# Kernel optimization log

Measured on AMD Instinct MI355X. Metric: run time of the kernel, lower is better.

Reference implementation:

```python
import jax, jax.numpy as jnp
import numpy as np

B, LA, LQ, LO, H, OUT = 32, 2048, 64, 32, 1024, 5


def _kaiming(key, out_f, in_f):
    return jax.random.normal(key, (out_f, in_f), jnp.float32) * np.sqrt(2.0 / in_f)


def setup_inputs() -> dict:
    key = jax.random.key(0)
    ks = jax.random.split(key, 16)
    inp = {
        "article_contexts": jax.random.normal(ks[0], (B, LA, H), jnp.float32),
        "question_contexts": jax.random.normal(ks[1], (B, LQ, H), jnp.float32),
        "options_embeds": jax.random.normal(ks[2], (B, 5, LO, H), jnp.float32),
        "answer_indices": jax.random.randint(ks[3], (B,), 0, LQ),
    }
    # mlp_att (article-question attention) params
    inp["a_Qw"], inp["a_Qb"] = _kaiming(ks[4], H, H), jnp.zeros((H,), jnp.float32)
    inp["a_Kw"], inp["a_Kb"] = _kaiming(ks[5], H, H), jnp.zeros((H,), jnp.float32)
    inp["a_Vw"], inp["a_Vb"] = _kaiming(ks[6], H, H), jnp.zeros((H,), jnp.float32)
    inp["a_vw"], inp["a_vb"] = _kaiming(ks[7], 1, H), jnp.zeros((1,), jnp.float32)
    # dot_layer (option attention) params
    inp["d_Qw"], inp["d_Qb"] = _kaiming(ks[8], H, H), jnp.zeros((H,), jnp.float32)
    inp["d_Kw"], inp["d_Kb"] = _kaiming(ks[9], H, H), jnp.zeros((H,), jnp.float32)
    inp["d_Vw"], inp["d_Vb"] = _kaiming(ks[10], H, H), jnp.zeros((H,), jnp.float32)
    inp["d_vw"], inp["d_vb"] = _kaiming(ks[11], 1, H), jnp.zeros((1,), jnp.float32)
    # final linear: hidden_size*5 -> output_dim
    inp["f_w"], inp["f_b"] = _kaiming(ks[12], OUT, 5 * H), jnp.zeros((OUT,), jnp.float32)
    return inp


def _mlp_att(Q, K, V, Qw, Qb, Kw, Kb, Vw, Vb, vw, vb):
    # Q: [B, H]; K, V: [B, (..opt..), L, H]. Dropout is identity (eval mode).
    Qp = Q @ Qw.T + Qb                      # [B, H]
    Kp = K @ Kw.T + Kb                      # [..., L, H]
    Vp = V @ Vw.T + Vb                      # [..., L, H]
    while Qp.ndim < Kp.ndim:
        Qp = Qp[..., None, :]
    M = jnp.tanh(Qp + Kp)                   # [..., L, H]
    scores = jax.nn.softmax(M @ vw.T + vb, axis=-2)  # softmax over L, [..., L, 1]
    return jnp.sum(Vp * scores, axis=-2)    # [..., H]


def reference(article_contexts, question_contexts, options_embeds, answer_indices,
              a_Qw, a_Qb, a_Kw, a_Kb, a_Vw, a_Vb, a_vw, a_vb,
              d_Qw, d_Qb, d_Kw, d_Kb, d_Vw, d_Vb, d_vw, d_vb,
              f_w, f_b):
    b = article_contexts.shape[0]
    # gather question context at the answer index -> [B, H]
    oqc = question_contexts[jnp.arange(b), answer_indices]
    # article-question additive attention -> [B, H]
    aq = _mlp_att(oqc, article_contexts, article_contexts,
                  a_Qw, a_Qb, a_Kw, a_Kb, a_Vw, a_Vb, a_vw, a_vb)
    # per-option additive attention, vectorized over the 5 options -> [B, 5, H]
    feats = _mlp_att(aq, options_embeds, options_embeds,
                     d_Qw, d_Qb, d_Kw, d_Kb, d_Vw, d_Vb, d_vw, d_vb)
    # concat options along feature dim, final linear -> [B, OUT]
    logits = feats.reshape(b, -1) @ f_w.T + f_b
    return logits
```

## Files before the change

kernel.cpp:

```cpp
#include <hip/hip_runtime.h>
#include <hip/hip_bf16.h>
#include <math.h>

#define HDIM 1024
#define NB 32
#define LA 2048
#define LO 32

typedef __attribute__((ext_vector_type(8))) short bf16x8;
typedef __attribute__((ext_vector_type(4))) float f32x4;
typedef unsigned int u32;

__device__ __forceinline__ float tanh_fast(float x){
    return 2.0f / (1.0f + __expf(-2.0f * x)) - 1.0f;
}

__device__ __forceinline__ void load_lds16(const void* gptr, void* lptr){
    __builtin_amdgcn_global_load_lds(
        (const __attribute__((address_space(1))) u32*)gptr,
        (__attribute__((address_space(3))) u32*)lptr, 16, 0, 0);
}

__global__ void zero_kernel(float* __restrict__ p, int n){
    int i = blockIdx.x * blockDim.x + threadIdx.x;
    int stride = gridDim.x * blockDim.x;
    for (; i < n; i += stride) p[i] = 0.0f;
}

__global__ void conv_bf16_kernel(const float* __restrict__ in, __hip_bfloat16* __restrict__ out, long n){
    long i = ((long)blockIdx.x * blockDim.x + threadIdx.x) * 4;
    long stride = (long)gridDim.x * blockDim.x * 4;
    for (; i < n; i += stride){
        float4 v = *(const float4*)(in + i);
        union { __hip_bfloat16 h[4]; short4 s; } u;
        u.h[0] = __float2bfloat16(v.x); u.h[1] = __float2bfloat16(v.y);
        u.h[2] = __float2bfloat16(v.z); u.h[3] = __float2bfloat16(v.w);
        *(short4*)(out + i) = u.s;
    }
}

__global__ void gather_kernel(const float* __restrict__ qc, const int* __restrict__ ans,
                              float* __restrict__ oqc){
    int b = blockIdx.x, tid = threadIdx.x;
    int idx = ans[b];
    const float* src = qc + ((size_t)b * 64 + idx) * HDIM;
    float* dst = oqc + (size_t)b * HDIM;
    #pragma unroll
    for (int l = 0; l < 4; l++) dst[tid + l * 256] = src[tid + l * 256];
}

__global__ __launch_bounds__(256) void proj_kernel(
    const float* __restrict__ in, const float* __restrict__ W,
    const float* __restrict__ bias, float* __restrict__ out){
    __shared__ float xin[HDIM];
    const int g = blockIdx.x, tid = threadIdx.x;
    const int lane = tid & 63, wave = tid >> 6;
    *(float4*)&xin[tid * 4] = *(const float4*)&in[(size_t)g * HDIM + tid * 4];
    __syncthreads();
    float4 xv[4];
    #pragma unroll
    for (int c = 0; c < 4; c++) xv[c] = *(const float4*)&xin[(c * 64 + lane) * 4];
    const int hbase = blockIdx.y * 64 + wave * 16;
    #pragma unroll 4
    for (int r = 0; r < 16; r++){
        int h = hbase + r;
        const float* Wr = W + (size_t)h * HDIM;
        float p = 0.f;
        #pragma unroll
        for (int c = 0; c < 4; c++){
            float4 wv = *(const float4*)&Wr[(c * 64 + lane) * 4];
            p = fmaf(xv[c].x, wv.x, p); p = fmaf(xv[c].y, wv.y, p);
            p = fmaf(xv[c].z, wv.z, p); p = fmaf(xv[c].w, wv.w, p);
        }
        #pragma unroll
        for (int off = 1; off < 64; off <<= 1) p += __shfl_xor(p, off, 64);
        if (lane == 0) out[(size_t)g * HDIM + h] = p + bias[h];
    }
}

#define NT 32
__global__ __launch_bounds__(512, 4) void score_mfma_kA(
    const __hip_bfloat16* __restrict__ X, const __hip_bfloat16* __restrict__ Kw,
    const float* __restrict__ Kb, const float* __restrict__ Qp,
    const float* __restrict__ vw, float* __restrict__ s,
    int row_off, int rows_per_batch)
{
    __shared__ __align__(16) char lds[49152];
    const int tid = threadIdx.x;
    const int lane = tid & 63, wid = tid >> 6;
    const int wm = wid >> 2, wn = wid & 3;
    const int lr = lane & 15, lg = lane >> 4;

    const int na = gridDim.x >> 3;
    const int per = na >> 3;
    const int bid = blockIdx.x;
    const int xcd = bid & 7, seq = bid >> 3;
    const int a_idx = xcd * per + (seq >> 3);
    const int h_idx = seq & 7;
    const int a0 = a_idx * 256;
    const int h0 = h_idx * 128;

    f32x4 acc[4][4] = {};

    const int rA  = tid >> 2;
    const int kcA = ((tid & 3) ^ ((rA >> 1) & 3)) * 16;
    const int rB1 = rA + 128;
    const char* pA  = (const char*)Kw + (size_t)(h0 + rA) * 2048 + kcA;
    const char* pB0 = (const char*)X  + (size_t)(a0 + rA) * 2048 + kcA;
    const char* pB1 = (const char*)X  + (size_t)(a0 + rB1) * 2048 + kcA;
    char* dA  = lds + tid * 16;
    char* dB0 = lds + 8192 + tid * 16;
    char* dB1 = lds + 16384 + tid * 16;

    int aoff[4], boff[4];
    #pragma unroll
    for (int hf = 0; hf < 4; hf++){
        int rw = wm * 64 + hf * 16 + lr;
        aoff[hf] = rw * 64 + ((lg * 16) ^ (((rw >> 1) & 3) << 4));
    }
    #pragma unroll
    for (int af = 0; af < 4; af++){
        int rw = wn * 64 + af * 16 + lr;
        boff[af] = 8192 + rw * 64 + ((lg * 16) ^ (((rw >> 1) & 3) << 4));
    }

#define STAGE_ADV(bufoff) do { \
    load_lds16(pA,  dA  + (bufoff)); \
    load_lds16(pB0, dB0 + (bufoff)); \
    load_lds16(pB1, dB1 + (bufoff)); \
    pA += 64; pB0 += 64; pB1 += 64; } while(0)

#define COMPUTE(bufoff) do { \
    bf16x8 av[4], bv[4]; \
    _Pragma("unroll") \
    for (int hf = 0; hf < 4; hf++) \
        av[hf] = *(const bf16x8*)(lds + (bufoff) + aoff[hf]); \
    _Pragma("unroll") \
    for (int af = 0; af < 4; af++) \
        bv[af] = *(const bf16x8*)(lds + (bufoff) + boff[af]); \
    __builtin_amdgcn_s_setprio(1); \
    _Pragma("unroll") \
    for (int hf = 0; hf < 4; hf++) \
        _Pragma("unroll") \
        for (int af = 0; af < 4; af++) \
            acc[hf][af] = __builtin_amdgcn_mfma_f32_16x16x32_bf16(av[hf], bv[af], acc[hf][af], 0, 0, 0); \
    __builtin_amdgcn_s_setprio(0); } while(0)

    STAGE_ADV(0);
    STAGE_ADV(24576);
    int bo = 0;
    for (int kt = 0; kt < NT - 1; ++kt){
        asm volatile("s_waitcnt vmcnt(3)" ::: "memory");
        __builtin_amdgcn_s_barrier();
        __builtin_amdgcn_sched_barrier(0);
        COMPUTE(bo);
        __builtin_amdgcn_s_barrier();
        if (kt < NT - 2) STAGE_ADV(bo);
        bo ^= 24576;
    }
    asm volatile("s_waitcnt vmcnt(0)" ::: "memory");
    __builtin_amdgcn_s_barrier();
    __builtin_amdgcn_sched_barrier(0);
    COMPUTE(bo);

    const int b = (row_off + a0) / rows_per_batch;
    float qv[4][4], vv[4][4];
    #pragma unroll
    for (int hf = 0; hf < 4; hf++){
        int hbase = h0 + wm * 64 + hf * 16 + lg * 4;
        float4 kb4 = *(const float4*)(Kb + hbase);
        float4 qp4 = *(const float4*)(Qp + (size_t)b * HDIM + hbase);
        float4 vw4 = *(const float4*)(vw + hbase);
        qv[hf][0] = kb4.x + qp4.x; qv[hf][1] = kb4.y + qp4.y;
        qv[hf][2] = kb4.z + qp4.z; qv[hf][3] = kb4.w + qp4.w;
        vv[hf][0] = vw4.x; vv[hf][1] = vw4.y; vv[hf][2] = vw4.z; vv[hf][3] = vw4.w;
    }
    #pragma unroll
    for (int af = 0; af < 4; af++){
        float sacc = 0.f;
        #pragma unroll
        for (int hf = 0; hf < 4; hf++)
            #pragma unroll
            for (int r = 0; r < 4; r++)
                sacc += tanh_fast(acc[hf][af][r] + qv[hf][r]) * vv[hf][r];
        sacc += __shfl_xor(sacc, 16, 64);
        sacc += __shfl_xor(sacc, 32, 64);
        if (lane < 16)
            atomicAdd(&s[row_off + a0 + wn * 64 + af * 16 + lr], sacc);
    }
#undef STAGE_ADV
#undef COMPUTE
}

#define SBM 128
#define SBN 128
__global__ __launch_bounds__(256) void score_mfma_kernel(
    const __hip_bfloat16* __restrict__ X, const __hip_bfloat16* __restrict__ Kw,
    const float* __restrict__ Kb, const float* __restrict__ Qp,
    const float* __restrict__ vw, float* __restrict__ s,
    int row_off, int rows_per_batch)
{
    __shared__ __align__(16) __hip_bfloat16 As[SBM][32];
    __shared__ __align__(16) __hip_bfloat16 Bs[SBN][32];
    const int tid = threadIdx.x;
    const int lane = tid & 63, wid = tid >> 6;
    const int wm = wid >> 1, wn = wid & 1;
    const int row0 = blockIdx.x * SBM;
    const int h0 = blockIdx.y * SBN;
    const int lr = lane & 15, lg = lane >> 4;

    f32x4 acc[4][4] = {};

    for (int k0 = 0; k0 < HDIM; k0 += 32){
        #pragma unroll
        for (int l = 0; l < 2; l++){
            int f = tid + l * 256;
            int r = f >> 2, c8 = (f & 3) * 8;
            load_lds16(X + (size_t)(row0 + r) * HDIM + k0 + c8, &As[0][0] + f * 8);
            load_lds16(Kw + (size_t)(h0 + r) * HDIM + k0 + c8, &Bs[0][0] + f * 8);
        }
        __syncthreads();
        bf16x8 a[4], b[4];
        #pragma unroll
        for (int i = 0; i < 4; i++)
            a[i] = *(const bf16x8*)&As[wm * 64 + i * 16 + lr][lg * 8];
        #pragma unroll
        for (int j = 0; j < 4; j++)
            b[j] = *(const bf16x8*)&Bs[wn * 64 + j * 16 + lr][lg * 8];
        #pragma unroll
        for (int i = 0; i < 4; i++)
            #pragma unroll
            for (int j = 0; j < 4; j++)
                acc[i][j] = __builtin_amdgcn_mfma_f32_16x16x32_bf16(a[i], b[j], acc[i][j], 0, 0, 0);
        __syncthreads();
    }

    float kbv[4], vwv[4];
    #pragma unroll
    for (int j = 0; j < 4; j++){
        int h = h0 + wn * 64 + j * 16 + lr;
        kbv[j] = Kb[h]; vwv[j] = vw[h];
    }
    #pragma unroll
    for (int i = 0; i < 4; i++){
        #pragma unroll
        for (int reg = 0; reg < 4; reg++){
            int r = row0 + wm * 64 + i * 16 + lg * 4 + reg;
            int gr = row_off + r;
            int bb = gr / rows_per_batch;
            const float* Qpb = Qp + (size_t)bb * HDIM;
            float p = 0.f;
            #pragma unroll
            for (int j = 0; j < 4; j++){
                int h = h0 + wn * 64 + j * 16 + lr;
                p += tanh_fast(acc[i][j][reg] + kbv[j] + Qpb[h]) * vwv[j];
            }
            #pragma unroll
            for (int off = 1; off < 16; off <<= 1) p += __shfl_xor(p, off, 16);
            if (lr == 0) atomicAdd(&s[gr], p);
        }
    }
}

__global__ void softmax_kernel(float* __restrict__ s, int Rg){
    __shared__ float red[4];
    int g = blockIdx.x, tid = threadIdx.x;
    float* sg = s + (size_t)g * Rg;
    float m = -INFINITY;
    for (int i = tid; i < Rg; i += 256) m = fmaxf(m, sg[i]);
    #pragma unroll
    for (int off = 32; off > 0; off >>= 1) m = fmaxf(m, __shfl_down(m, off, 64));
    if ((tid & 63) == 0) red[tid >> 6] = m;
    __syncthreads();
    m = fmaxf(fmaxf(red[0], red[1]), fmaxf(red[2], red[3]));
    __syncthreads();
    float sum = 0.f;
    for (int i = tid; i < Rg; i += 256){ float e = __expf(sg[i] - m); sg[i] = e; sum += e; }
    #pragma unroll
    for (int off = 32; off > 0; off >>= 1) sum += __shfl_down(sum, off, 64);
    if ((tid & 63) == 0) red[tid >> 6] = sum;
    __syncthreads();
    float inv = 1.0f / (red[0] + red[1] + red[2] + red[3]);
    for (int i = tid; i < Rg; i += 256) sg[i] *= inv;
}

__global__ void wsum_kernel(const float* __restrict__ X, const float* __restrict__ sc,
                            float* __restrict__ out, int Rg, int rowsPerChunk){
    __shared__ float scs[256];
    int g = blockIdx.x >> 2;
    int kc = blockIdx.x & 3;
    int i0 = blockIdx.y * rowsPerChunk;
    int tid = threadIdx.x;
    if (tid < rowsPerChunk) scs[tid] = sc[(size_t)g * Rg + i0 + tid];
    __syncthreads();
    int k = kc * 256 + tid;
    const float* Xg = X + ((size_t)g * Rg + i0) * HDIM + k;
    float acc = 0.f;
    for (int i = 0; i < rowsPerChunk; i++)
        acc += scs[i] * Xg[(size_t)i * HDIM];
    atomicAdd(&out[(size_t)g * HDIM + k], acc);
}

__global__ void wsum_bf16_kernel(const __hip_bfloat16* __restrict__ X, const float* __restrict__ sc,
                                 float* __restrict__ out, int Rg, int rowsPerChunk){
    __shared__ float scs[256];
    int g = blockIdx.x >> 2;
    int kc = blockIdx.x & 3;
    int i0 = blockIdx.y * rowsPerChunk;
    int tid = threadIdx.x;
    if (tid < rowsPerChunk) scs[tid] = sc[(size_t)g * Rg + i0 + tid];
    __syncthreads();
    int k = kc * 256 + tid;
    const __hip_bfloat16* Xg = X + ((size_t)g * Rg + i0) * HDIM + k;
    float acc = 0.f;
    for (int i = 0; i < rowsPerChunk; i++)
        acc += scs[i] * __bfloat162float(Xg[(size_t)i * HDIM]);
    atomicAdd(&out[(size_t)g * HDIM + k], acc);
}

__global__ void final_kernel(const float* __restrict__ feats, const float* __restrict__ fw,
                             const float* __restrict__ fb, float* __restrict__ out){
    __shared__ float red[4];
    int b = blockIdx.x, tid = threadIdx.x;
    const float* fe = feats + (size_t)b * 5120;
    for (int j = 0; j < 5; j++){
        float acc = 0.f;
        for (int i = tid; i < 5120; i += 256) acc += fe[i] * fw[(size_t)j * 5120 + i];
        #pragma unroll
        for (int off = 32; off > 0; off >>= 1) acc += __shfl_down(acc, off, 64);
        if ((tid & 63) == 0) red[tid >> 6] = acc;
        __syncthreads();
        if (tid == 0) out[b * 5 + j] = fb[j] + red[0] + red[1] + red[2] + red[3];
        __syncthreads();
    }
}

extern "C" void kernel_launch(void* const* d_in, const int* in_sizes, int n_in,
                              void* d_out, int out_size, void* d_ws, size_t ws_size,
                              hipStream_t stream) {
    const float* article  = (const float*)d_in[0];
    const float* question = (const float*)d_in[1];
    const float* options  = (const float*)d_in[2];
    const int*   ans      = (const int*)d_in[3];
    const float* a_Qw = (const float*)d_in[4];  const float* a_Qb = (const float*)d_in[5];
    const float* a_Kw = (const float*)d_in[6];  const float* a_Kb = (const float*)d_in[7];
    const float* a_Vw = (const float*)d_in[8];  const float* a_Vb = (const float*)d_in[9];
    const float* a_vw = (const float*)d_in[10];
    const float* d_Qw = (const float*)d_in[12]; const float* d_Qb = (const float*)d_in[13];
    const float* d_Kw = (const float*)d_in[14]; const float* d_Kb = (const float*)d_in[15];
    const float* d_Vw = (const float*)d_in[16]; const float* d_Vb = (const float*)d_in[17];
    const float* d_vw = (const float*)d_in[18];
    const float* f_w  = (const float*)d_in[20]; const float* f_b  = (const float*)d_in[21];
    float* out = (float*)d_out;

    float* ws = (float*)d_ws;
    float* oqc   = ws;
    float* qp_a  = ws + 32768;
    float* aq    = ws + 65536;
    float* qp_d  = ws + 98304;
    float* feats = ws + 131072;
    float* s_art = ws + 294912;
    float* s_opt = ws + 360448;
    float* w_art = ws + 365568;
    float* wd    = ws + 398336;
    __hip_bfloat16* kwa_bf = (__hip_bfloat16*)(ws + 562176);
    __hip_bfloat16* kwd_bf = kwa_bf + 1048576;
    __hip_bfloat16* opt_bf = kwd_bf + 1048576;
    __hip_bfloat16* art_bf = opt_bf + 5242880;
    size_t used_bytes = 562176 * 4 + (size_t)(1048576 * 2 + 5242880) * 2;
    long avail_rows = (long)((ws_size - used_bytes) / (HDIM * 2));
    int rows_total = NB * LA;
    int chunk_rows = (int)(avail_rows < rows_total ? avail_rows : rows_total);
    chunk_rows &= ~2047;
    if (chunk_rows < 2048) chunk_rows = 2048;

    zero_kernel<<<256, 256, 0, stream>>>(s_art, 267264);
    gather_kernel<<<NB, 256, 0, stream>>>(question, ans, oqc);
    proj_kernel<<<dim3(NB, 16), 256, 0, stream>>>(oqc, a_Qw, a_Qb, qp_a);
    conv_bf16_kernel<<<64, 256, 0, stream>>>(a_Kw, kwa_bf, 1048576);

    for (int r0 = 0; r0 < rows_total; r0 += chunk_rows){
        int nr = rows_total - r0; if (nr > chunk_rows) nr = chunk_rows;
        conv_bf16_kernel<<<1024, 256, 0, stream>>>(article + (size_t)r0 * HDIM, art_bf, (long)nr * HDIM);
        score_mfma_kA<<<(nr / 256) * 8, 512, 0, stream>>>(
            art_bf, kwa_bf, a_Kb, qp_a, a_vw, s_art, r0, LA);
    }
    softmax_kernel<<<NB, 256, 0, stream>>>(s_art, LA);
    if (chunk_rows >= rows_total)
        wsum_bf16_kernel<<<dim3(NB * 4, 8), 256, 0, stream>>>(art_bf, s_art, w_art, LA, 256);
    else
        wsum_kernel<<<dim3(NB * 4, 8), 256, 0, stream>>>(article, s_art, w_art, LA, 256);
    proj_kernel<<<dim3(NB, 16), 256, 0, stream>>>(w_art, a_Vw, a_Vb, aq);

    proj_kernel<<<dim3(NB, 16), 256, 0, stream>>>(aq, d_Qw, d_Qb, qp_d);
    conv_bf16_kernel<<<64, 256, 0, stream>>>(d_Kw, kwd_bf, 1048576);
    conv_bf16_kernel<<<320, 256, 0, stream>>>(options, opt_bf, 5242880);
    score_mfma_kernel<<<dim3((NB * 5 * LO) / SBM, HDIM / SBN), 256, 0, stream>>>(
        opt_bf, kwd_bf, d_Kb, qp_d, d_vw, s_opt, 0, 5 * LO);
    softmax_kernel<<<NB * 5, 256, 0, stream>>>(s_opt, LO);
    wsum_kernel<<<dim3(NB * 5 * 4, 1), 256, 0, stream>>>(options, s_opt, wd, LO, LO);
    proj_kernel<<<dim3(NB * 5, 16), 256, 0, stream>>>(wd, d_Vw, d_Vb, feats);
    final_kernel<<<NB, 256, 0, stream>>>(feats, f_w, f_b, out);
}
```

Measured before the change: 446.2 us.

## Enlarge article score GEMM tile to 256x256 with deeper 8-phase pipelined LDS staging

The article-score MFMA kernel now computes 256 hidden by 256 row tiles per block instead of 128 by 256, halving the grid and the number of times each article row is re-read from global memory. The K loop is restructured into a multi-stage, 8-phase schedule over 128 KB of LDS. Loads for two 32-wide k slabs are interleaved with split LDS reads and MFMA groups, with fine-grained vmcnt waits and barriers. This raises arithmetic intensity and overlaps loads with compute, at the cost of more registers, more LDS, fewer resident blocks per CU, and a more fragile hand-tuned schedule.

After: 439.4 us. Within noise of the previous version (-1.5%).

```diff
diff --git a/kernel.cpp b/kernel.cpp
--- a/kernel.cpp
+++ b/kernel.cpp
@@ -78,118 +78,144 @@
     }
 }
 
-#define NT 32
-__global__ __launch_bounds__(512, 4) void score_mfma_kA(
+__global__ __launch_bounds__(512, 2) void score_mfma8p(
     const __hip_bfloat16* __restrict__ X, const __hip_bfloat16* __restrict__ Kw,
     const float* __restrict__ Kb, const float* __restrict__ Qp,
     const float* __restrict__ vw, float* __restrict__ s,
     int row_off, int rows_per_batch)
 {
-    __shared__ __align__(16) char lds[49152];
+    __shared__ __align__(16) char lds[131072];
     const int tid = threadIdx.x;
     const int lane = tid & 63, wid = tid >> 6;
     const int wm = wid >> 2, wn = wid & 3;
     const int lr = lane & 15, lg = lane >> 4;
 
-    const int na = gridDim.x >> 3;
-    const int per = na >> 3;
+    const int na = gridDim.x >> 2;
     const int bid = blockIdx.x;
     const int xcd = bid & 7, seq = bid >> 3;
-    const int a_idx = xcd * per + (seq >> 3);
-    const int h_idx = seq & 7;
-    const int a0 = a_idx * 256;
-    const int h0 = h_idx * 128;
-
-    f32x4 acc[4][4] = {};
-
-    const int rA  = tid >> 2;
-    const int kcA = ((tid & 3) ^ ((rA >> 1) & 3)) * 16;
-    const int rB1 = rA + 128;
-    const char* pA  = (const char*)Kw + (size_t)(h0 + rA) * 2048 + kcA;
-    const char* pB0 = (const char*)X  + (size_t)(a0 + rA) * 2048 + kcA;
-    const char* pB1 = (const char*)X  + (size_t)(a0 + rB1) * 2048 + kcA;
-    char* dA  = lds + tid * 16;
-    char* dB0 = lds + 8192 + tid * 16;
-    char* dB1 = lds + 16384 + tid * 16;
-
-    int aoff[4], boff[4];
-    #pragma unroll
-    for (int hf = 0; hf < 4; hf++){
-        int rw = wm * 64 + hf * 16 + lr;
+    const int a_idx = xcd * (na >> 3) + (seq >> 2);
+    const int h_idx = seq & 3;
+    const int a0 = a_idx * 256, h0 = h_idx * 256;
+
+    f32x4 acc[8][4] = {};
+    bf16x8 av[8], bv[4];
+
+    const int rA = tid >> 2;
+    const int csw = ((tid & 3) * 16) ^ (((rA >> 1) & 3) << 4);
+    const char* pA = (const char*)Kw + (size_t)(h0 + rA) * 2048 + csw;
+    const char* pB = (const char*)X  + (size_t)(a0 + rA) * 2048 + csw;
+    char* dst0 = lds + tid * 16;
+
+    int aoff[8], boff[4];
+    #pragma unroll
+    for (int hf = 0; hf < 8; hf++){
+        int rw = wm * 128 + hf * 16 + lr;
         aoff[hf] = rw * 64 + ((lg * 16) ^ (((rw >> 1) & 3) << 4));
     }
     #pragma unroll
     for (int af = 0; af < 4; af++){
         int rw = wn * 64 + af * 16 + lr;
-        boff[af] = 8192 + rw * 64 + ((lg * 16) ^ (((rw >> 1) & 3) << 4));
-    }
-
-#define STAGE_ADV(bufoff) do { \
-    load_lds16(pA,  dA  + (bufoff)); \
-    load_lds16(pB0, dB0 + (bufoff)); \
-    load_lds16(pB1, dB1 + (bufoff)); \
-    pA += 64; pB0 += 64; pB1 += 64; } while(0)
-
-#define COMPUTE(bufoff) do { \
-    bf16x8 av[4], bv[4]; \
+        boff[af] = 16384 + rw * 64 + ((lg * 16) ^ (((rw >> 1) & 3) << 4));
+    }
+
+#define ISSUE(P, KOFF, SLOT, PLANE) do { \
+    load_lds16((P) + (KOFF), dst0 + (SLOT) + (PLANE)); \
+    load_lds16((P) + (KOFF) + 262144, dst0 + (SLOT) + (PLANE) + 8192); } while(0)
+#define READS_A(BASE) do { \
     _Pragma("unroll") \
-    for (int hf = 0; hf < 4; hf++) \
-        av[hf] = *(const bf16x8*)(lds + (bufoff) + aoff[hf]); \
+    for (int hf = 0; hf < 8; hf++) av[hf] = *(const bf16x8*)(lds + (BASE) + aoff[hf]); \
+    bv[0] = *(const bf16x8*)(lds + (BASE) + boff[0]); \
+    bv[1] = *(const bf16x8*)(lds + (BASE) + boff[1]); } while(0)
+#define READS_B(BASE) do { \
+    bv[2] = *(const bf16x8*)(lds + (BASE) + boff[2]); \
+    bv[3] = *(const bf16x8*)(lds + (BASE) + boff[3]); } while(0)
+#define MFMA2(A0, A1) do { __builtin_amdgcn_s_setprio(1); \
     _Pragma("unroll") \
-    for (int af = 0; af < 4; af++) \
-        bv[af] = *(const bf16x8*)(lds + (bufoff) + boff[af]); \
-    __builtin_amdgcn_s_setprio(1); \
-    _Pragma("unroll") \
-    for (int hf = 0; hf < 4; hf++) \
-        _Pragma("unroll") \
-        for (int af = 0; af < 4; af++) \
-            acc[hf][af] = __builtin_amdgcn_mfma_f32_16x16x32_bf16(av[hf], bv[af], acc[hf][af], 0, 0, 0); \
+    for (int hf = 0; hf < 8; hf++){ \
+        acc[hf][A0] = __builtin_amdgcn_mfma_f32_16x16x32_bf16(av[hf], bv[A0], acc[hf][A0], 0, 0, 0); \
+        acc[hf][A1] = __builtin_amdgcn_mfma_f32_16x16x32_bf16(av[hf], bv[A1], acc[hf][A1], 0, 0, 0); } \
     __builtin_amdgcn_s_setprio(0); } while(0)
-
-    STAGE_ADV(0);
-    STAGE_ADV(24576);
-    int bo = 0;
-    for (int kt = 0; kt < NT - 1; ++kt){
-        asm volatile("s_waitcnt vmcnt(3)" ::: "memory");
-        __builtin_amdgcn_s_barrier();
-        __builtin_amdgcn_sched_barrier(0);
-        COMPUTE(bo);
-        __builtin_amdgcn_s_barrier();
-        if (kt < NT - 2) STAGE_ADV(bo);
-        bo ^= 24576;
-    }
-    asm volatile("s_waitcnt vmcnt(0)" ::: "memory");
-    __builtin_amdgcn_s_barrier();
-    __builtin_amdgcn_sched_barrier(0);
-    COMPUTE(bo);
+#define BAR() __builtin_amdgcn_s_barrier()
+
+    ISSUE(pA, 0, 0, 0);        ISSUE(pB, 0, 0, 16384);
+    ISSUE(pA, 64, 0, 32768);   ISSUE(pB, 64, 0, 49152);
+    ISSUE(pA, 128, 65536, 0);  ISSUE(pB, 128, 65536, 16384);
+
+    for (int t = 0; t < 14; ++t){
+        const int st = (t & 1) << 16;
+        const int so = st ^ 65536;
+        const int kb = t * 128;
+        ISSUE(pA, kb + 192, so, 32768);
+        asm volatile("s_waitcnt vmcnt(10)" ::: "memory");
+        BAR();
+        READS_A(st);
+        BAR();
+        MFMA2(0, 1);
+        ISSUE(pB, kb + 192, so, 49152);
+        READS_B(st);
+        BAR();
+        MFMA2(2, 3);
+        ISSUE(pA, kb + 256, st, 0);
+        asm volatile("s_waitcnt vmcnt(10)" ::: "memory");
+        BAR();
+        READS_A(st + 32768);
+        BAR();
+        MFMA2(0, 1);
+        ISSUE(pB, kb + 256, st, 16384);
+        READS_B(st + 32768);
+        BAR();
+        MFMA2(2, 3);
+    }
+    {
+        ISSUE(pA, 14 * 128 + 192, 65536, 32768);
+        asm volatile("s_waitcnt vmcnt(10)" ::: "memory");
+        BAR(); READS_A(0); BAR(); MFMA2(0, 1);
+        ISSUE(pB, 14 * 128 + 192, 65536, 49152);
+        READS_B(0); BAR(); MFMA2(2, 3);
+        asm volatile("s_waitcnt vmcnt(8)" ::: "memory");
+        BAR(); READS_A(32768); BAR(); MFMA2(0, 1);
+        READS_B(32768); BAR(); MFMA2(2, 3);
+    }
+    {
+        asm volatile("s_waitcnt vmcnt(4)" ::: "memory");
+        BAR(); READS_A(65536); BAR(); MFMA2(0, 1);
+        READS_B(65536); BAR(); MFMA2(2, 3);
+        asm volatile("s_waitcnt vmcnt(0)" ::: "memory");
+        BAR(); READS_A(65536 + 32768); BAR(); MFMA2(0, 1);
+        READS_B(65536 + 32768); BAR(); MFMA2(2, 3);
+    }
 
     const int b = (row_off + a0) / rows_per_batch;
-    float qv[4][4], vv[4][4];
-    #pragma unroll
-    for (int hf = 0; hf < 4; hf++){
-        int hbase = h0 + wm * 64 + hf * 16 + lg * 4;
+    float part[4] = {0.f, 0.f, 0.f, 0.f};
+    #pragma unroll
+    for (int hf = 0; hf < 8; hf++){
+        int hbase = h0 + wm * 128 + hf * 16 + lg * 4;
         float4 kb4 = *(const float4*)(Kb + hbase);
         float4 qp4 = *(const float4*)(Qp + (size_t)b * HDIM + hbase);
         float4 vw4 = *(const float4*)(vw + hbase);
-        qv[hf][0] = kb4.x + qp4.x; qv[hf][1] = kb4.y + qp4.y;
-        qv[hf][2] = kb4.z + qp4.z; qv[hf][3] = kb4.w + qp4.w;
-        vv[hf][0] = vw4.x; vv[hf][1] = vw4.y; vv[hf][2] = vw4.z; vv[hf][3] = vw4.w;
+        float q0v = kb4.x + qp4.x, q1v = kb4.y + qp4.y;
+        float q2v = kb4.z + qp4.z, q3v = kb4.w + qp4.w;
+        #pragma unroll
+        for (int af = 0; af < 4; af++){
+            part[af] += tanh_fast(acc[hf][af][0] + q0v) * vw4.x;
+            part[af] += tanh_fast(acc[hf][af][1] + q1v) * vw4.y;
+            part[af] += tanh_fast(acc[hf][af][2] + q2v) * vw4.z;
+            part[af] += tanh_fast(acc[hf][af][3] + q3v) * vw4.w;
+        }
     }
     #pragma unroll
     for (int af = 0; af < 4; af++){
-        float sacc = 0.f;
-        #pragma unroll
-        for (int hf = 0; hf < 4; hf++)
-            #pragma unroll
-            for (int r = 0; r < 4; r++)
-                sacc += tanh_fast(acc[hf][af][r] + qv[hf][r]) * vv[hf][r];
-        sacc += __shfl_xor(sacc, 16, 64);
-        sacc += __shfl_xor(sacc, 32, 64);
+        float p = part[af];
+        p += __shfl_xor(p, 16, 64);
+        p += __shfl_xor(p, 32, 64);
         if (lane < 16)
-            atomicAdd(&s[row_off + a0 + wn * 64 + af * 16 + lr], sacc);
-    }
-#undef STAGE_ADV
-#undef COMPUTE
+            atomicAdd(&s[row_off + a0 + wn * 64 + af * 16 + lr], p);
+    }
+#undef ISSUE
+#undef READS_A
+#undef READS_B
+#undef MFMA2
+#undef BAR
 }
 
 #define SBM 128
@@ -382,7 +408,7 @@
     for (int r0 = 0; r0 < rows_total; r0 += chunk_rows){
         int nr = rows_total - r0; if (nr > chunk_rows) nr = chunk_rows;
         conv_bf16_kernel<<<1024, 256, 0, stream>>>(article + (size_t)r0 * HDIM, art_bf, (long)nr * HDIM);
-        score_mfma_kA<<<(nr / 256) * 8, 512, 0, stream>>>(
+        score_mfma8p<<<(nr / 256) * 4, 512, 0, stream>>>(
             art_bf, kwa_bf, a_Kb, qp_a, a_vw, s_art, r0, LA);
     }
     softmax_kernel<<<NB, 256, 0, stream>>>(s_art, LA);
```

## Fuse fp32-to-bf16 article conversion into score MFMA kernel load path

Applied to the files above, without the earlier changes.

The article score GEMM now reads fp32 activations directly, converting them to bf16 in registers and writing them to swizzled LDS. This replaces the separate conversion pass and the bf16 staging buffer. The aim is to avoid writing and re-reading a 128MB bf16 copy and to drop the chunking loop. The trade-off is that B loads go through registers with a full vmcnt(0) wait each iteration instead of async direct-to-LDS loads, which weakens the pipelining. wsum also now reads fp32 from the article instead of the bf16 copy, which doubles its read traffic.

New measurement: 490.0 us. +9.8%, slower.

```diff
diff --git a/kernel.cpp b/kernel.cpp
--- a/kernel.cpp
+++ b/kernel.cpp
@@ -79,11 +79,11 @@
 }
 
 #define NT 32
-__global__ __launch_bounds__(512, 4) void score_mfma_kA(
-    const __hip_bfloat16* __restrict__ X, const __hip_bfloat16* __restrict__ Kw,
+__global__ __launch_bounds__(512, 4) void score_mfma_f32b(
+    const float* __restrict__ Xf, const __hip_bfloat16* __restrict__ Kw,
     const float* __restrict__ Kb, const float* __restrict__ Qp,
     const float* __restrict__ vw, float* __restrict__ s,
-    int row_off, int rows_per_batch)
+    int rows_per_batch)
 {
     __shared__ __align__(16) char lds[49152];
     const int tid = threadIdx.x;
@@ -92,25 +92,25 @@
     const int lr = lane & 15, lg = lane >> 4;
 
     const int na = gridDim.x >> 3;
-    const int per = na >> 3;
     const int bid = blockIdx.x;
     const int xcd = bid & 7, seq = bid >> 3;
-    const int a_idx = xcd * per + (seq >> 3);
+    const int a_idx = xcd * (na >> 3) + (seq >> 3);
     const int h_idx = seq & 7;
-    const int a0 = a_idx * 256;
-    const int h0 = h_idx * 128;
+    const int a0 = a_idx * 256, h0 = h_idx * 128;
 
     f32x4 acc[4][4] = {};
 
-    const int rA  = tid >> 2;
-    const int kcA = ((tid & 3) ^ ((rA >> 1) & 3)) * 16;
-    const int rB1 = rA + 128;
-    const char* pA  = (const char*)Kw + (size_t)(h0 + rA) * 2048 + kcA;
-    const char* pB0 = (const char*)X  + (size_t)(a0 + rA) * 2048 + kcA;
-    const char* pB1 = (const char*)X  + (size_t)(a0 + rB1) * 2048 + kcA;
-    char* dA  = lds + tid * 16;
-    char* dB0 = lds + 8192 + tid * 16;
-    char* dB1 = lds + 16384 + tid * 16;
+    const int rA = tid >> 2;
+    const int srcbA = ((tid & 3) * 16) ^ (((rA >> 1) & 3) << 4);
+    const char* pA = (const char*)Kw + (size_t)(h0 + rA) * 2048 + srcbA;
+    char* dA = lds + tid * 16;
+
+    const int rB = tid >> 1;
+    const int hb = tid & 1;
+    const float* pB = Xf + (size_t)(a0 + rB) * HDIM + hb * 16;
+    const int swzB = ((rB >> 1) & 3) << 4;
+    char* dB0 = lds + 8192 + rB * 64 + ((hb * 32) ^ swzB);
+    char* dB1 = lds + 8192 + rB * 64 + ((hb * 32 + 16) ^ swzB);
 
     int aoff[4], boff[4];
     #pragma unroll
@@ -124,20 +124,29 @@
         boff[af] = 8192 + rw * 64 + ((lg * 16) ^ (((rw >> 1) & 3) << 4));
     }
 
-#define STAGE_ADV(bufoff) do { \
-    load_lds16(pA,  dA  + (bufoff)); \
-    load_lds16(pB0, dB0 + (bufoff)); \
-    load_lds16(pB1, dB1 + (bufoff)); \
-    pA += 64; pB0 += 64; pB1 += 64; } while(0)
-
+    float4 br0, br1, br2, br3;
+#define LOADB(kt) do { const float* q = pB + (kt) * 32; \
+    br0 = *(const float4*)q; br1 = *(const float4*)(q + 4); \
+    br2 = *(const float4*)(q + 8); br3 = *(const float4*)(q + 12); } while(0)
+#define CVTWRITE(bufoff) do { \
+    union { __hip_bfloat16 h[8]; bf16x8 v; } u0, u1; \
+    u0.h[0]=__float2bfloat16(br0.x); u0.h[1]=__float2bfloat16(br0.y); \
+    u0.h[2]=__float2bfloat16(br0.z); u0.h[3]=__float2bfloat16(br0.w); \
+    u0.h[4]=__float2bfloat16(br1.x); u0.h[5]=__float2bfloat16(br1.y); \
+    u0.h[6]=__float2bfloat16(br1.z); u0.h[7]=__float2bfloat16(br1.w); \
+    u1.h[0]=__float2bfloat16(br2.x); u1.h[1]=__float2bfloat16(br2.y); \
+    u1.h[2]=__float2bfloat16(br2.z); u1.h[3]=__float2bfloat16(br2.w); \
+    u1.h[4]=__float2bfloat16(br3.x); u1.h[5]=__float2bfloat16(br3.y); \
+    u1.h[6]=__float2bfloat16(br3.z); u1.h[7]=__float2bfloat16(br3.w); \
+    *(bf16x8*)(dB0 + (bufoff)) = u0.v; \
+    *(bf16x8*)(dB1 + (bufoff)) = u1.v; } while(0)
+#define ISSUEA(kt, bufoff) load_lds16(pA + (size_t)(kt) * 64, dA + (bufoff))
 #define COMPUTE(bufoff) do { \
     bf16x8 av[4], bv[4]; \
     _Pragma("unroll") \
-    for (int hf = 0; hf < 4; hf++) \
-        av[hf] = *(const bf16x8*)(lds + (bufoff) + aoff[hf]); \
+    for (int hf = 0; hf < 4; hf++) av[hf] = *(const bf16x8*)(lds + (bufoff) + aoff[hf]); \
     _Pragma("unroll") \
-    for (int af = 0; af < 4; af++) \
-        bv[af] = *(const bf16x8*)(lds + (bufoff) + boff[af]); \
+    for (int af = 0; af < 4; af++) bv[af] = *(const bf16x8*)(lds + (bufoff) + boff[af]); \
     __builtin_amdgcn_s_setprio(1); \
     _Pragma("unroll") \
     for (int hf = 0; hf < 4; hf++) \
@@ -146,24 +155,28 @@
             acc[hf][af] = __builtin_amdgcn_mfma_f32_16x16x32_bf16(av[hf], bv[af], acc[hf][af], 0, 0, 0); \
     __builtin_amdgcn_s_setprio(0); } while(0)
 
-    STAGE_ADV(0);
-    STAGE_ADV(24576);
+    ISSUEA(0, 0);
+    LOADB(0);
+    CVTWRITE(0);
+    asm volatile("s_waitcnt vmcnt(0)" ::: "memory");
+    __syncthreads();
+
     int bo = 0;
-    for (int kt = 0; kt < NT - 1; ++kt){
-        asm volatile("s_waitcnt vmcnt(3)" ::: "memory");
-        __builtin_amdgcn_s_barrier();
-        __builtin_amdgcn_sched_barrier(0);
+    for (int t = 0; t < NT; ++t){
+        if (t < NT - 1){
+            ISSUEA(t + 1, bo ^ 24576);
+            LOADB(t + 1);
+        }
         COMPUTE(bo);
-        __builtin_amdgcn_s_barrier();
-        if (kt < NT - 2) STAGE_ADV(bo);
+        if (t < NT - 1){
+            CVTWRITE(bo ^ 24576);
+            asm volatile("s_waitcnt vmcnt(0)" ::: "memory");
+        }
+        __syncthreads();
         bo ^= 24576;
     }
-    asm volatile("s_waitcnt vmcnt(0)" ::: "memory");
-    __builtin_amdgcn_s_barrier();
-    __builtin_amdgcn_sched_barrier(0);
-    COMPUTE(bo);
-
-    const int b = (row_off + a0) / rows_per_batch;
+
+    const int b = a0 / rows_per_batch;
     float qv[4][4], vv[4][4];
     #pragma unroll
     for (int hf = 0; hf < 4; hf++){
@@ -186,9 +199,11 @@
         sacc += __shfl_xor(sacc, 16, 64);
         sacc += __shfl_xor(sacc, 32, 64);
         if (lane < 16)
-            atomicAdd(&s[row_off + a0 + wn * 64 + af * 16 + lr], sacc);
-    }
-#undef STAGE_ADV
+            atomicAdd(&s[a0 + wn * 64 + af * 16 + lr], sacc);
+    }
+#undef LOADB
+#undef CVTWRITE
+#undef ISSUEA
 #undef COMPUTE
 }
 
@@ -298,23 +313,6 @@
     float acc = 0.f;
     for (int i = 0; i < rowsPerChunk; i++)
         acc += scs[i] * Xg[(size_t)i * HDIM];
-    atomicAdd(&out[(size_t)g * HDIM + k], acc);
-}
-
-__global__ void wsum_bf16_kernel(const __hip_bfloat16* __restrict__ X, const float* __restrict__ sc,
-                                 float* __restrict__ out, int Rg, int rowsPerChunk){
-    __shared__ float scs[256];
-    int g = blockIdx.x >> 2;
-    int kc = blockIdx.x & 3;
-    int i0 = blockIdx.y * rowsPerChunk;
-    int tid = threadIdx.x;
-    if (tid < rowsPerChunk) scs[tid] = sc[(size_t)g * Rg + i0 + tid];
-    __syncthreads();
-    int k = kc * 256 + tid;
-    const __hip_bfloat16* Xg = X + ((size_t)g * Rg + i0) * HDIM + k;
-    float acc = 0.f;
-    for (int i = 0; i < rowsPerChunk; i++)
-        acc += scs[i] * __bfloat162float(Xg[(size_t)i * HDIM]);
     atomicAdd(&out[(size_t)g * HDIM + k], acc);
 }
 
@@ -366,30 +364,16 @@
     __hip_bfloat16* kwa_bf = (__hip_bfloat16*)(ws + 562176);
     __hip_bfloat16* kwd_bf = kwa_bf + 1048576;
     __hip_bfloat16* opt_bf = kwd_bf + 1048576;
-    __hip_bfloat16* art_bf = opt_bf + 5242880;
-    size_t used_bytes = 562176 * 4 + (size_t)(1048576 * 2 + 5242880) * 2;
-    long avail_rows = (long)((ws_size - used_bytes) / (HDIM * 2));
-    int rows_total = NB * LA;
-    int chunk_rows = (int)(avail_rows < rows_total ? avail_rows : rows_total);
-    chunk_rows &= ~2047;
-    if (chunk_rows < 2048) chunk_rows = 2048;
 
     zero_kernel<<<256, 256, 0, stream>>>(s_art, 267264);
     gather_kernel<<<NB, 256, 0, stream>>>(question, ans, oqc);
     proj_kernel<<<dim3(NB, 16), 256, 0, stream>>>(oqc, a_Qw, a_Qb, qp_a);
     conv_bf16_kernel<<<64, 256, 0, stream>>>(a_Kw, kwa_bf, 1048576);
 
-    for (int r0 = 0; r0 < rows_total; r0 += chunk_rows){
-        int nr = rows_total - r0; if (nr > chunk_rows) nr = chunk_rows;
-        conv_bf16_kernel<<<1024, 256, 0, stream>>>(article + (size_t)r0 * HDIM, art_bf, (long)nr * HDIM);
-        score_mfma_kA<<<(nr / 256) * 8, 512, 0, stream>>>(
-            art_bf, kwa_bf, a_Kb, qp_a, a_vw, s_art, r0, LA);
-    }
+    score_mfma_f32b<<<(NB * LA / 256) * 8, 512, 0, stream>>>(
+        article, kwa_bf, a_Kb, qp_a, a_vw, s_art, LA);
     softmax_kernel<<<NB, 256, 0, stream>>>(s_art, LA);
-    if (chunk_rows >= rows_total)
-        wsum_bf16_kernel<<<dim3(NB * 4, 8), 256, 0, stream>>>(art_bf, s_art, w_art, LA, 256);
-    else
-        wsum_kernel<<<dim3(NB * 4, 8), 256, 0, stream>>>(article, s_art, w_art, LA, 256);
+    wsum_kernel<<<dim3(NB * 4, 8), 256, 0, stream>>>(article, s_art, w_art, LA, 256);
     proj_kernel<<<dim3(NB, 16), 256, 0, stream>>>(w_art, a_Vw, a_Vb, aq);
 
     proj_kernel<<<dim3(NB, 16), 256, 0, stream>>>(aq, d_Qw, d_Qb, qp_d);
```
